# Kernel optimization log

Measured on AMD Instinct MI355X. Metric: run time of the kernel, lower is better.

Reference implementation:

```python
import jax, jax.numpy as jnp
import numpy as np

B, T, H, W, C = 8, 16, 64, 64, 16
HID = 64  # hidden_dim of each ConvLSTM cell
K = 3     # kernel size


def _convlstm_step(x, h, c, Wk, b):
    # conv over concat([x, h]) -> 4*HID gate channels (i, f, o, g)
    z = jax.lax.conv_general_dilated(
        jnp.concatenate([x, h], axis=-1), Wk,
        window_strides=(1, 1), padding='SAME',
        dimension_numbers=('NHWC', 'HWIO', 'NHWC')) + b
    i, f, o, g = jnp.split(z, 4, axis=-1)
    c_new = jax.nn.sigmoid(f) * c + jax.nn.sigmoid(i) * jnp.tanh(g)
    h_new = jax.nn.sigmoid(o) * jnp.tanh(c_new)
    return h_new, c_new


def setup_inputs() -> dict:
    key = jax.random.key(0)
    k1, k2, k3 = jax.random.split(key, 3)
    enc_input = jax.random.normal(k1, (B, T, H, W, C), jnp.float32)
    # input cell: in_channels = C + HID; stacked hidden cell: 2*HID
    W0 = jax.random.normal(k2, (K, K, C + HID, 4 * HID), jnp.float32) * 0.05
    b0 = jnp.zeros((4 * HID,), jnp.float32)
    W1 = jax.random.normal(k3, (K, K, 2 * HID, 4 * HID), jnp.float32) * 0.05
    b1 = jnp.zeros((4 * HID,), jnp.float32)
    return {"enc_input": enc_input, "W0": W0, "b0": b0, "W1": W1, "b1": b1}


def reference(enc_input, W0, b0, W1, b1):
    Bv, Tv, Hv, Wv, _ = enc_input.shape
    z0 = jnp.zeros((Bv, Hv, Wv, HID), enc_input.dtype)

    def step(carry, x_t):
        h0, c0, h1, c1 = carry
        h0, c0 = _convlstm_step(x_t, h0, c0, W0, b0)   # input ConvLSTM
        h1, c1 = _convlstm_step(h0, h1, c1, W1, b1)    # stacked hidden ConvLSTM
        return (h0, c0, h1, c1), None

    xs = jnp.moveaxis(enc_input, 1, 0)  # [T, B, H, W, C]
    (h0, c0, h1, c1), _ = jax.lax.scan(step, (z0, z0, z0, z0), xs)
    # Encoder returns last hidden layer's (h, c)
    return (h1, c1)
```

## Files before the change

kernel.cpp:

```cpp
#include <hip/hip_runtime.h>
#include <hip/hip_bf16.h>

#define Bv 8
#define Tv 16
#define Hv 64
#define Wv 64
#define Cv 16
#define HID 64
#define PH 66

typedef short short8 __attribute__((ext_vector_type(8)));
typedef float f32x4 __attribute__((ext_vector_type(4)));
typedef unsigned short u16x8 __attribute__((ext_vector_type(8)));

__device__ __forceinline__ unsigned short f2bf(float x) {
  union { float f; unsigned int u; } v; v.f = x;
  unsigned int r = v.u + 0x7FFF + ((v.u >> 16) & 1);
  return (unsigned short)(r >> 16);
}
__device__ __forceinline__ float sigmoid_f(float x) {
  return 1.f / (1.f + __expf(-x));
}
__device__ __forceinline__ float tanh_f(float x) {
  float e = __expf(2.f * x);
  return 1.f - 2.f / (e + 1.f);
}

__global__ void init_all(const float* __restrict__ enc,
                         const float* __restrict__ W0, const float* __restrict__ W1,
                         unsigned short* __restrict__ h0a, unsigned short* __restrict__ h0b,
                         unsigned short* __restrict__ h1a, unsigned short* __restrict__ h1b,
                         unsigned short* __restrict__ xb0, unsigned short* __restrict__ xb1,
                         unsigned short* __restrict__ w0r, unsigned short* __restrict__ w1r)
{
  const int gb = blockIdx.x, tid = threadIdx.x;
  if (gb < 293) {
    int idx = gb * 256 + tid;
    u16x8 z = {};
    if (idx < 8320) {
      int bufi = idx / 4160, rem = idx - bufi * 4160;
      int b = rem / 520, r2 = rem - b * 520;
      int hp = r2 >> 1, c8 = r2 & 1;
      int y, x;
      if (hp < 66)       { y = 0;  x = hp; }
      else if (hp < 132) { y = 65; x = hp - 66; }
      else { int i2 = hp - 132; y = 1 + (i2 >> 1); x = (i2 & 1) * 65; }
      unsigned short* base = bufi ? xb1 : xb0;
      *(u16x8*)(base + ((size_t)((b * PH + y) * PH) + x) * 16 + c8 * 8) = z;
      return;
    }
    idx -= 8320;
    int bufi = idx / 16640;
    if (bufi >= 4) return;
    int rem = idx - bufi * 16640;
    int b = rem / 2080, r2 = rem - b * 2080;
    int hp = r2 >> 3, c8 = r2 & 7;
    int y, x;
    if (hp < 66)       { y = 0;  x = hp; }
    else if (hp < 132) { y = 65; x = hp - 66; }
    else { int i2 = hp - 132; y = 1 + (i2 >> 1); x = (i2 & 1) * 65; }
    unsigned short* base = (bufi == 0) ? h0a : (bufi == 1) ? h0b : (bufi == 2) ? h1a : h1b;
    *(u16x8*)(base + ((size_t)((b * PH + y) * PH) + x) * 64 + c8 * 8) = z;
  } else if (gb < 1029) {
    int o = (gb - 293) * 256 + tid;
    if (o >= 23 * 8192) return;
    int cc = o >> 13, t = o & 8191;
    int wn = t >> 11, t2 = t & 2047;
    int g = t2 >> 9, t3 = t2 & 511;
    int l = t3 >> 3, e = t3 & 7;
    int kg = l >> 4, r = l & 15;
    int k = kg * 8 + e;
    int col = g * 64 + wn * 16 + r;
    float v = 0.f;
    if (cc < 4) {
      int tap = 2 * cc + (k >> 4);
      v = W0[(size_t)(tap * 80 + (k & 15)) * 256 + col];
    } else if (cc == 4) {
      if (k < 16) v = W0[(size_t)(8 * 80 + k) * 256 + col];
    } else {
      int hcc = cc - 5, tap = hcc >> 1, cgi = hcc & 1;
      v = W0[(size_t)(tap * 80 + 16 + cgi * 32 + k) * 256 + col];
    }
    w0r[o] = f2bf(v);
  } else if (gb < 2181) {
    int o = (gb - 1029) * 256 + tid;
    if (o >= 36 * 8192) return;
    int cc = o >> 13, t = o & 8191;
    int wn = t >> 11, t2 = t & 2047;
    int g = t2 >> 9, t3 = t2 & 511;
    int l = t3 >> 3, e = t3 & 7;
    int kg = l >> 4, r = l & 15;
    int k = kg * 8 + e;
    int col = g * 64 + wn * 16 + r;
    int tap = cc >> 2, cgi = cc & 3;
    w1r[o] = f2bf(W1[(size_t)(tap * 128 + cgi * 32 + k) * 256 + col]);
  } else {
    int idx = (gb - 2181) * 256 + tid;
    int b = idx >> 12, pix = idx & 4095;
    int y = pix >> 6, x = pix & 63;
    const float* s = enc + ((size_t)(b * Tv + 0) * 4096 + pix) * 16;
    float4 f0 = *(const float4*)(s);
    float4 f1 = *(const float4*)(s + 4);
    float4 f2 = *(const float4*)(s + 8);
    float4 f3 = *(const float4*)(s + 12);
    u16x8 o0, o1;
    o0[0]=f2bf(f0.x); o0[1]=f2bf(f0.y); o0[2]=f2bf(f0.z); o0[3]=f2bf(f0.w);
    o0[4]=f2bf(f1.x); o0[5]=f2bf(f1.y); o0[6]=f2bf(f1.z); o0[7]=f2bf(f1.w);
    o1[0]=f2bf(f2.x); o1[1]=f2bf(f2.y); o1[2]=f2bf(f2.z); o1[3]=f2bf(f2.w);
    o1[4]=f2bf(f3.x); o1[5]=f2bf(f3.y); o1[6]=f2bf(f3.z); o1[7]=f2bf(f3.w);
    unsigned short* d = xb0 + ((size_t)((b * PH + y + 1) * PH) + (x + 1)) * 16;
    *(u16x8*)(d)     = o0;
    *(u16x8*)(d + 8) = o1;
  }
}

template<int CELL, int NC>
__device__ __forceinline__ void cell_run(
    const char* __restrict__ A0, const char* __restrict__ A1,
    const char* __restrict__ Wr, const float* __restrict__ bias,
    float* __restrict__ cbuf, unsigned short* __restrict__ hout,
    float* __restrict__ h1fin, float* __restrict__ c1fin,
    char* lds, int b, int by, int bx, int tid)
{
  constexpr bool T0C = (CELL == 0) ? (NC == 5) : (NC == 18);
  const int l = tid & 63, w = tid >> 6;
  const int wm = w >> 2, wn = w & 3;
  const int r = l & 15, kg = l >> 4;
  const int j = wn * 16 + r;

  char* ldsA = lds;
  char* ldsW = lds + 3 * 8192;

  int pixs;
  {
    int ps = w * 16 + r;
    int ys = by * 16 + (ps >> 3), xs = bx * 8 + (ps & 7);
    pixs = (b * PH + ys) * PH + xs;
  }
  const int zpix = b * PH * PH;

  auto ISSUE_A = [&](int cc, int buf) {
    char* dst = ldsA + buf * 8192;
    if constexpr (CELL == 0) {
      if (cc < 5) {
        int tapA = 2 * cc;
        int kyA = tapA / 3, kxA = tapA - kyA * 3;
        unsigned offA = (unsigned)((pixs + kyA * PH + kxA) * 32 + kg * 16);
        unsigned offB;
        if (cc < 4) {
          int tapB = tapA + 1;
          int kyB = tapB / 3, kxB = tapB - kyB * 3;
          offB = (unsigned)((pixs + kyB * PH + kxB) * 32 + (kg - 2) * 16);
        } else {
          offB = (unsigned)(zpix * 32 + (kg - 2) * 16);
        }
        unsigned aoff = (kg < 2) ? offA : offB;
        __builtin_amdgcn_global_load_lds((const unsigned int*)(A0 + aoff),
                                         (unsigned int*)(dst + w * 1024), 16, 0, 0);
      } else {
        int hcc = cc - 5, tap = hcc >> 1, cgi = hcc & 1;
        int ky = tap / 3, kx = tap - ky * 3;
        unsigned aoff = (unsigned)((pixs + ky * PH + kx) * 128 + cgi * 64 + kg * 16);
        __builtin_amdgcn_global_load_lds((const unsigned int*)(A1 + aoff),
                                         (unsigned int*)(dst + w * 1024), 16, 0, 0);
      }
    } else {
      int tap, cgi;
      if (T0C) { tap = cc >> 1; cgi = cc & 1; }
      else     { tap = cc >> 2; cgi = cc & 3; }
      int ky = tap / 3, kx = tap - ky * 3;
      const char* srcb = (cgi < 2) ? A0 : A1;
      unsigned aoff = (unsigned)((pixs + ky * PH + kx) * 128 + (cgi & 1) * 64 + kg * 16);
      __builtin_amdgcn_global_load_lds((const unsigned int*)(srcb + aoff),
                                       (unsigned int*)(dst + w * 1024), 16, 0, 0);
    }
  };

  auto ISSUE_W = [&](int cc, int buf) {
    char* dst = ldsW + buf * 16384;
    int wcc;
    if constexpr (CELL == 0) wcc = cc;
    else                     wcc = T0C ? ((cc >> 1) * 4 + (cc & 1)) : cc;
    const char* wp = Wr + (size_t)wcc * 16384 + (unsigned)(w * 2048 + l * 16);
    __builtin_amdgcn_global_load_lds((const unsigned int*)(wp),
                                     (unsigned int*)(dst + w * 2048), 16, 0, 0);
    __builtin_amdgcn_global_load_lds((const unsigned int*)(wp + 1024),
                                     (unsigned int*)(dst + w * 2048 + 1024), 16, 0, 0);
  };

  f32x4 acc[4][4] = {};
  short8 af[4], bfv[4];

  ISSUE_W(0, 0);
  __builtin_amdgcn_sched_barrier(0);
  ISSUE_A(0, 0);
  __builtin_amdgcn_sched_barrier(0);
  ISSUE_A(1, 1);
  __builtin_amdgcn_sched_barrier(0);

#pragma unroll
  for (int cc = 0; cc < NC; ++cc) {
    if (cc == NC - 1) { asm volatile("s_waitcnt vmcnt(0)" ::: "memory"); }
    else              { asm volatile("s_waitcnt vmcnt(1)" ::: "memory"); }
    __builtin_amdgcn_sched_barrier(0);
    __builtin_amdgcn_s_barrier();
    __builtin_amdgcn_sched_barrier(0);

    if (cc + 1 < NC) ISSUE_W(cc + 1, (cc + 1) & 1);
    __builtin_amdgcn_sched_barrier(0);
    if (cc + 2 < NC) ISSUE_A(cc + 2, (cc + 2) % 3);

    const char* bufA = ldsA + (cc % 3) * 8192;
    const char* bufW = ldsW + (cc & 1) * 16384;
#pragma unroll
    for (int mi = 0; mi < 4; ++mi)
      af[mi] = *(const short8*)(bufA + (wm * 4 + mi) * 1024 + l * 16);
#pragma unroll
    for (int g = 0; g < 4; ++g)
      bfv[g] = *(const short8*)(bufW + (wn * 4 + g) * 1024 + l * 16);

    __builtin_amdgcn_s_setprio(1);
#pragma unroll
    for (int mi = 0; mi < 4; ++mi)
#pragma unroll
      for (int g = 0; g < 4; ++g)
        acc[mi][g] = __builtin_amdgcn_mfma_f32_16x16x32_bf16(
            af[mi], bfv[g], acc[mi][g], 0, 0, 0);
    __builtin_amdgcn_s_setprio(0);
  }

  float bi[4];
#pragma unroll
  for (int g = 0; g < 4; ++g) bi[g] = bias[g * 64 + j];
  float cpre[4][4];
#pragma unroll
  for (int mi = 0; mi < 4; ++mi) {
#pragma unroll
    for (int rg = 0; rg < 4; ++rg) {
      if constexpr (T0C) { cpre[mi][rg] = 0.f; }
      else {
        int p = wm * 64 + mi * 16 + kg * 4 + rg;
        int y = by * 16 + (p >> 3), x = bx * 8 + (p & 7);
        cpre[mi][rg] = cbuf[((size_t)((b * Hv + y) * Wv) + x) * HID + j];
      }
    }
  }
#pragma unroll
  for (int mi = 0; mi < 4; ++mi) {
#pragma unroll
    for (int rg = 0; rg < 4; ++rg) {
      int p = wm * 64 + mi * 16 + kg * 4 + rg;
      int y = by * 16 + (p >> 3), x = bx * 8 + (p & 7);
      float zi = acc[mi][0][rg] + bi[0];
      float zf = acc[mi][1][rg] + bi[1];
      float zo = acc[mi][2][rg] + bi[2];
      float zg = acc[mi][3][rg] + bi[3];
      float cn = sigmoid_f(zf) * cpre[mi][rg] + sigmoid_f(zi) * tanh_f(zg);
      float hn = sigmoid_f(zo) * tanh_f(cn);
      size_t ci = ((size_t)((b * Hv + y) * Wv) + x) * HID + j;
      cbuf[ci] = cn;
      hout[((size_t)((b * PH + y + 1) * PH) + (x + 1)) * HID + j] = f2bf(hn);
      if (CELL == 1 && h1fin != nullptr) {
        h1fin[ci] = hn;
        c1fin[ci] = cn;
      }
    }
  }
}

template<int NC1, int NC0, bool LAST>
__global__ __launch_bounds__(512, 4)
void step_fused(const unsigned short* __restrict__ xbr, unsigned short* __restrict__ xbw,
                const unsigned short* __restrict__ h0r, unsigned short* __restrict__ h0w,
                const unsigned short* __restrict__ h1r, unsigned short* __restrict__ h1w,
                const unsigned short* __restrict__ w0r, const unsigned short* __restrict__ w1r,
                const float* __restrict__ b0, const float* __restrict__ b1,
                float* __restrict__ c0, float* __restrict__ c1,
                float* __restrict__ h1f, float* __restrict__ c1f,
                const float* __restrict__ enc, int tnext)
{
  extern __shared__ char lds[];
  const int tid = threadIdx.x;
  const int gid = blockIdx.x;
  int isC1, k;
  if constexpr (NC1 > 0 && NC0 > 0) { isC1 = (gid < 256) ? 1 : 0; k = gid & 255; }
  else if constexpr (NC1 > 0)       { isC1 = 1; k = gid; }
  else                              { isC1 = 0; k = gid; }
  const int b = k >> 5, rem = k & 31;
  const int by = rem >> 3, bx = rem & 7;

  if constexpr (NC1 > 0) {
    if (isC1) {
      cell_run<1, NC1>((const char*)h0r, (const char*)h1r, (const char*)w1r, b1,
                       c1, h1w, LAST ? h1f : nullptr, LAST ? c1f : nullptr,
                       lds, b, by, bx, tid);
      return;
    }
  }
  if constexpr (NC0 > 0) {
    cell_run<0, NC0>((const char*)xbr, (const char*)h0r, (const char*)w0r, b0,
                     c0, h0w, nullptr, nullptr, lds, b, by, bx, tid);
    if (tnext >= 0) {
      int pp = tid >> 2, q4 = tid & 3;
      int y = by * 16 + (pp >> 3), x = bx * 8 + (pp & 7);
      const float* s = enc + ((size_t)(b * Tv + tnext) * 4096 + (y * 64 + x)) * 16 + q4 * 4;
      float4 f = *(const float4*)s;
      unsigned short* d = xbw + ((size_t)((b * PH + y + 1) * PH) + (x + 1)) * 16 + q4 * 4;
      d[0] = f2bf(f.x); d[1] = f2bf(f.y); d[2] = f2bf(f.z); d[3] = f2bf(f.w);
    }
  }
}

extern "C" void kernel_launch(void* const* d_in, const int* in_sizes, int n_in,
                              void* d_out, int out_size, void* d_ws, size_t ws_size,
                              hipStream_t stream) {
  const float* enc = (const float*)d_in[0];
  const float* W0  = (const float*)d_in[1];
  const float* b0  = (const float*)d_in[2];
  const float* W1  = (const float*)d_in[3];
  const float* b1  = (const float*)d_in[4];

  float* out = (float*)d_out;
  const size_t NST = (size_t)Bv * Hv * Wv * HID;
  float* h1f = out;
  float* c1  = out + NST;

  char* ws = (char*)d_ws;
  const size_t SZ_C = NST * 4;
  const size_t SZ_H = (size_t)Bv * PH * PH * HID * 2;
  const size_t SZ_X = (size_t)Bv * PH * PH * 16 * 2;
  float*          c0  = (float*)ws;
  unsigned short* h0a = (unsigned short*)(ws + SZ_C);
  unsigned short* h0b = (unsigned short*)(ws + SZ_C + SZ_H);
  unsigned short* h1a = (unsigned short*)(ws + SZ_C + 2 * SZ_H);
  unsigned short* h1b = (unsigned short*)(ws + SZ_C + 3 * SZ_H);
  unsigned short* xb0 = (unsigned short*)(ws + SZ_C + 4 * SZ_H);
  unsigned short* xb1 = (unsigned short*)(ws + SZ_C + 4 * SZ_H + SZ_X);
  unsigned short* w0r = (unsigned short*)(ws + SZ_C + 4 * SZ_H + 2 * SZ_X);
  unsigned short* w1r = (unsigned short*)(ws + SZ_C + 4 * SZ_H + 2 * SZ_X + (size_t)23 * 16384);

  hipFuncSetAttribute((const void*)step_fused<0,5,false>,   hipFuncAttributeMaxDynamicSharedMemorySize, 65536);
  hipFuncSetAttribute((const void*)step_fused<18,23,false>, hipFuncAttributeMaxDynamicSharedMemorySize, 65536);
  hipFuncSetAttribute((const void*)step_fused<36,23,false>, hipFuncAttributeMaxDynamicSharedMemorySize, 65536);
  hipFuncSetAttribute((const void*)step_fused<36,0,true>,   hipFuncAttributeMaxDynamicSharedMemorySize, 65536);

  init_all<<<2309, 256, 0, stream>>>(enc, W0, W1, h0a, h0b, h1a, h1b,
                                     xb0, xb1, w0r, w1r);

  const int LDSB = 57344;
  step_fused<0,5,false><<<256, 512, LDSB, stream>>>(
      xb0, xb1, h0b, h0a, h1a, h1b, w0r, w1r, b0, b1, c0, c1,
      nullptr, nullptr, enc, 1);
  for (int t = 1; t <= 15; ++t) {
    unsigned short* h0r = (t & 1) ? h0a : h0b;
    unsigned short* h0w = (t & 1) ? h0b : h0a;
    unsigned short* h1r = (t & 1) ? h1b : h1a;
    unsigned short* h1w = (t & 1) ? h1a : h1b;
    unsigned short* xr  = (t & 1) ? xb1 : xb0;
    unsigned short* xw  = (t & 1) ? xb0 : xb1;
    int tn = (t + 1 <= 15) ? (t + 1) : -1;
    if (t == 1)
      step_fused<18,23,false><<<512, 512, LDSB, stream>>>(
          xr, xw, h0r, h0w, h1r, h1w, w0r, w1r, b0, b1, c0, c1,
          nullptr, nullptr, enc, tn);
    else
      step_fused<36,23,false><<<512, 512, LDSB, stream>>>(
          xr, xw, h0r, h0w, h1r, h1w, w0r, w1r, b0, b1, c0, c1,
          nullptr, nullptr, enc, tn);
  }
  step_fused<36,0,true><<<256, 512, LDSB, stream>>>(
      xb0, xb1, h0b, h0a, h1a, h1b, w0r, w1r, b0, b1, c0, c1,
      h1f, c1, enc, -1);
}
```

Measured before the change: 604.1 us.

## Process two K-chunks per pipeline stage in stacked cell to halve barriers

Splits the cell routine into separate input-cell and hidden-cell versions. The hidden-cell version loads and computes two 32-channel chunks per pipeline stage with triple buffering, halving the number of barriers and waitcnt points per tap. This requires much larger LDS staging buffers, so the dynamic shared memory for every launch grows to 144 KB. That likely limits each CU to a single block and reduces latency hiding for both cells.

New measurement: 705.5 us. 16.8% more time.

```diff
diff --git a/kernel.cpp b/kernel.cpp
--- a/kernel.cpp
+++ b/kernel.cpp
@@ -114,15 +114,14 @@
   }
 }
 
-template<int CELL, int NC>
-__device__ __forceinline__ void cell_run(
+template<int NC>
+__device__ __forceinline__ void cell0_run(
     const char* __restrict__ A0, const char* __restrict__ A1,
     const char* __restrict__ Wr, const float* __restrict__ bias,
     float* __restrict__ cbuf, unsigned short* __restrict__ hout,
-    float* __restrict__ h1fin, float* __restrict__ c1fin,
     char* lds, int b, int by, int bx, int tid)
 {
-  constexpr bool T0C = (CELL == 0) ? (NC == 5) : (NC == 18);
+  constexpr bool T0C = (NC == 5);
   const int l = tid & 63, w = tid >> 6;
   const int wm = w >> 2, wn = w & 3;
   const int r = l & 15, kg = l >> 4;
@@ -141,47 +140,33 @@
 
   auto ISSUE_A = [&](int cc, int buf) {
     char* dst = ldsA + buf * 8192;
-    if constexpr (CELL == 0) {
-      if (cc < 5) {
-        int tapA = 2 * cc;
-        int kyA = tapA / 3, kxA = tapA - kyA * 3;
-        unsigned offA = (unsigned)((pixs + kyA * PH + kxA) * 32 + kg * 16);
-        unsigned offB;
-        if (cc < 4) {
-          int tapB = tapA + 1;
-          int kyB = tapB / 3, kxB = tapB - kyB * 3;
-          offB = (unsigned)((pixs + kyB * PH + kxB) * 32 + (kg - 2) * 16);
-        } else {
-          offB = (unsigned)(zpix * 32 + (kg - 2) * 16);
-        }
-        unsigned aoff = (kg < 2) ? offA : offB;
-        __builtin_amdgcn_global_load_lds((const unsigned int*)(A0 + aoff),
-                                         (unsigned int*)(dst + w * 1024), 16, 0, 0);
+    if (cc < 5) {
+      int tapA = 2 * cc;
+      int kyA = tapA / 3, kxA = tapA - kyA * 3;
+      unsigned offA = (unsigned)((pixs + kyA * PH + kxA) * 32 + kg * 16);
+      unsigned offB;
+      if (cc < 4) {
+        int tapB = tapA + 1;
+        int kyB = tapB / 3, kxB = tapB - kyB * 3;
+        offB = (unsigned)((pixs + kyB * PH + kxB) * 32 + (kg - 2) * 16);
       } else {
-        int hcc = cc - 5, tap = hcc >> 1, cgi = hcc & 1;
-        int ky = tap / 3, kx = tap - ky * 3;
-        unsigned aoff = (unsigned)((pixs + ky * PH + kx) * 128 + cgi * 64 + kg * 16);
-        __builtin_amdgcn_global_load_lds((const unsigned int*)(A1 + aoff),
-                                         (unsigned int*)(dst + w * 1024), 16, 0, 0);
+        offB = (unsigned)(zpix * 32 + (kg - 2) * 16);
       }
+      unsigned aoff = (kg < 2) ? offA : offB;
+      __builtin_amdgcn_global_load_lds((const unsigned int*)(A0 + aoff),
+                                       (unsigned int*)(dst + w * 1024), 16, 0, 0);
     } else {
-      int tap, cgi;
-      if (T0C) { tap = cc >> 1; cgi = cc & 1; }
-      else     { tap = cc >> 2; cgi = cc & 3; }
+      int hcc = cc - 5, tap = hcc >> 1, cgi = hcc & 1;
       int ky = tap / 3, kx = tap - ky * 3;
-      const char* srcb = (cgi < 2) ? A0 : A1;
-      unsigned aoff = (unsigned)((pixs + ky * PH + kx) * 128 + (cgi & 1) * 64 + kg * 16);
-      __builtin_amdgcn_global_load_lds((const unsigned int*)(srcb + aoff),
+      unsigned aoff = (unsigned)((pixs + ky * PH + kx) * 128 + cgi * 64 + kg * 16);
+      __builtin_amdgcn_global_load_lds((const unsigned int*)(A1 + aoff),
                                        (unsigned int*)(dst + w * 1024), 16, 0, 0);
     }
   };
 
   auto ISSUE_W = [&](int cc, int buf) {
     char* dst = ldsW + buf * 16384;
-    int wcc;
-    if constexpr (CELL == 0) wcc = cc;
-    else                     wcc = T0C ? ((cc >> 1) * 4 + (cc & 1)) : cc;
-    const char* wp = Wr + (size_t)wcc * 16384 + (unsigned)(w * 2048 + l * 16);
+    const char* wp = Wr + (size_t)cc * 16384 + (unsigned)(w * 2048 + l * 16);
     __builtin_amdgcn_global_load_lds((const unsigned int*)(wp),
                                      (unsigned int*)(dst + w * 2048), 16, 0, 0);
     __builtin_amdgcn_global_load_lds((const unsigned int*)(wp + 1024),
@@ -260,7 +245,126 @@
       size_t ci = ((size_t)((b * Hv + y) * Wv) + x) * HID + j;
       cbuf[ci] = cn;
       hout[((size_t)((b * PH + y + 1) * PH) + (x + 1)) * HID + j] = f2bf(hn);
-      if (CELL == 1 && h1fin != nullptr) {
+    }
+  }
+}
+
+template<int NC>
+__device__ __forceinline__ void cell1_run(
+    const char* __restrict__ A0, const char* __restrict__ A1,
+    const char* __restrict__ Wr, const float* __restrict__ bias,
+    float* __restrict__ cbuf, unsigned short* __restrict__ hout,
+    float* __restrict__ h1fin, float* __restrict__ c1fin,
+    char* lds, int b, int by, int bx, int tid)
+{
+  constexpr bool T0C = (NC == 18);
+  constexpr int NP = NC / 2;
+  const int l = tid & 63, w = tid >> 6;
+  const int wm = w >> 2, wn = w & 3;
+  const int r = l & 15, kg = l >> 4;
+  const int j = wn * 16 + r;
+
+  char* ldsA = lds;
+  char* ldsW = lds + 3 * 16384;
+
+  int pixs;
+  {
+    int ps = w * 16 + r;
+    int ys = by * 16 + (ps >> 3), xs = bx * 8 + (ps & 7);
+    pixs = (b * PH + ys) * PH + xs;
+  }
+
+  auto ISSUE = [&](int p, int buf) {
+    int tap, ss;
+    if (T0C) { tap = p; ss = 0; } else { tap = p >> 1; ss = p & 1; }
+    int ky = tap / 3, kx = tap - ky * 3;
+    const char* srcb = ss ? A1 : A0;
+    unsigned abase = (unsigned)((pixs + ky * PH + kx) * 128 + kg * 16);
+    char* dstA = ldsA + buf * 16384 + w * 1024;
+#pragma unroll
+    for (int hh = 0; hh < 2; ++hh)
+      __builtin_amdgcn_global_load_lds((const unsigned int*)(srcb + abase + hh * 64),
+                                       (unsigned int*)(dstA + hh * 8192), 16, 0, 0);
+    int wbase = tap * 4 + 2 * ss;
+    const char* wp = Wr + (size_t)wbase * 16384 + (unsigned)(w * 4096 + l * 16);
+    char* dstW = ldsW + buf * 32768 + w * 4096;
+#pragma unroll
+    for (int q = 0; q < 4; ++q)
+      __builtin_amdgcn_global_load_lds((const unsigned int*)(wp + q * 1024),
+                                       (unsigned int*)(dstW + q * 1024), 16, 0, 0);
+  };
+
+  f32x4 acc[4][4] = {};
+  short8 af[4], bfv[4];
+
+  ISSUE(0, 0);
+  __builtin_amdgcn_sched_barrier(0);
+  ISSUE(1, 1);
+  __builtin_amdgcn_sched_barrier(0);
+
+#pragma unroll
+  for (int p = 0; p < NP; ++p) {
+    if (p <= NP - 2) { asm volatile("s_waitcnt vmcnt(6)" ::: "memory"); }
+    else             { asm volatile("s_waitcnt vmcnt(0)" ::: "memory"); }
+    __builtin_amdgcn_sched_barrier(0);
+    __builtin_amdgcn_s_barrier();
+    __builtin_amdgcn_sched_barrier(0);
+
+    if (p + 2 < NP) ISSUE(p + 2, (p + 2) % 3);
+
+    const char* bufA = ldsA + (p % 3) * 16384;
+    const char* bufW = ldsW + (p % 3) * 32768;
+#pragma unroll
+    for (int s = 0; s < 2; ++s) {
+#pragma unroll
+      for (int mi = 0; mi < 4; ++mi)
+        af[mi] = *(const short8*)(bufA + s * 8192 + (wm * 4 + mi) * 1024 + l * 16);
+#pragma unroll
+      for (int g = 0; g < 4; ++g)
+        bfv[g] = *(const short8*)(bufW + s * 16384 + (wn * 4 + g) * 1024 + l * 16);
+      __builtin_amdgcn_s_setprio(1);
+#pragma unroll
+      for (int mi = 0; mi < 4; ++mi)
+#pragma unroll
+        for (int g = 0; g < 4; ++g)
+          acc[mi][g] = __builtin_amdgcn_mfma_f32_16x16x32_bf16(
+              af[mi], bfv[g], acc[mi][g], 0, 0, 0);
+      __builtin_amdgcn_s_setprio(0);
+    }
+  }
+
+  float bi[4];
+#pragma unroll
+  for (int g = 0; g < 4; ++g) bi[g] = bias[g * 64 + j];
+  float cpre[4][4];
+#pragma unroll
+  for (int mi = 0; mi < 4; ++mi) {
+#pragma unroll
+    for (int rg = 0; rg < 4; ++rg) {
+      if constexpr (T0C) { cpre[mi][rg] = 0.f; }
+      else {
+        int p = wm * 64 + mi * 16 + kg * 4 + rg;
+        int y = by * 16 + (p >> 3), x = bx * 8 + (p & 7);
+        cpre[mi][rg] = cbuf[((size_t)((b * Hv + y) * Wv) + x) * HID + j];
+      }
+    }
+  }
+#pragma unroll
+  for (int mi = 0; mi < 4; ++mi) {
+#pragma unroll
+    for (int rg = 0; rg < 4; ++rg) {
+      int p = wm * 64 + mi * 16 + kg * 4 + rg;
+      int y = by * 16 + (p >> 3), x = bx * 8 + (p & 7);
+      float zi = acc[mi][0][rg] + bi[0];
+      float zf = acc[mi][1][rg] + bi[1];
+      float zo = acc[mi][2][rg] + bi[2];
+      float zg = acc[mi][3][rg] + bi[3];
+      float cn = sigmoid_f(zf) * cpre[mi][rg] + sigmoid_f(zi) * tanh_f(zg);
+      float hn = sigmoid_f(zo) * tanh_f(cn);
+      size_t ci = ((size_t)((b * Hv + y) * Wv) + x) * HID + j;
+      cbuf[ci] = cn;
+      hout[((size_t)((b * PH + y + 1) * PH) + (x + 1)) * HID + j] = f2bf(hn);
+      if (h1fin != nullptr) {
         h1fin[ci] = hn;
         c1fin[ci] = cn;
       }
@@ -291,15 +395,15 @@
 
   if constexpr (NC1 > 0) {
     if (isC1) {
-      cell_run<1, NC1>((const char*)h0r, (const char*)h1r, (const char*)w1r, b1,
-                       c1, h1w, LAST ? h1f : nullptr, LAST ? c1f : nullptr,
-                       lds, b, by, bx, tid);
+      cell1_run<NC1>((const char*)h0r, (const char*)h1r, (const char*)w1r, b1,
+                     c1, h1w, LAST ? h1f : nullptr, LAST ? c1f : nullptr,
+                     lds, b, by, bx, tid);
       return;
     }
   }
   if constexpr (NC0 > 0) {
-    cell_run<0, NC0>((const char*)xbr, (const char*)h0r, (const char*)w0r, b0,
-                     c0, h0w, nullptr, nullptr, lds, b, by, bx, tid);
+    cell0_run<NC0>((const char*)xbr, (const char*)h0r, (const char*)w0r, b0,
+                   c0, h0w, lds, b, by, bx, tid);
     if (tnext >= 0) {
       int pp = tid >> 2, q4 = tid & 3;
       int y = by * 16 + (pp >> 3), x = bx * 8 + (pp & 7);
@@ -339,15 +443,15 @@
   unsigned short* w0r = (unsigned short*)(ws + SZ_C + 4 * SZ_H + 2 * SZ_X);
   unsigned short* w1r = (unsigned short*)(ws + SZ_C + 4 * SZ_H + 2 * SZ_X + (size_t)23 * 16384);
 
-  hipFuncSetAttribute((const void*)step_fused<0,5,false>,   hipFuncAttributeMaxDynamicSharedMemorySize, 65536);
-  hipFuncSetAttribute((const void*)step_fused<18,23,false>, hipFuncAttributeMaxDynamicSharedMemorySize, 65536);
-  hipFuncSetAttribute((const void*)step_fused<36,23,false>, hipFuncAttributeMaxDynamicSharedMemorySize, 65536);
-  hipFuncSetAttribute((const void*)step_fused<36,0,true>,   hipFuncAttributeMaxDynamicSharedMemorySize, 65536);
+  hipFuncSetAttribute((const void*)step_fused<0,5,false>,   hipFuncAttributeMaxDynamicSharedMemorySize, 147456);
+  hipFuncSetAttribute((const void*)step_fused<18,23,false>, hipFuncAttributeMaxDynamicSharedMemorySize, 147456);
+  hipFuncSetAttribute((const void*)step_fused<36,23,false>, hipFuncAttributeMaxDynamicSharedMemorySize, 147456);
+  hipFuncSetAttribute((const void*)step_fused<36,0,true>,   hipFuncAttributeMaxDynamicSharedMemorySize, 147456);
 
   init_all<<<2309, 256, 0, stream>>>(enc, W0, W1, h0a, h0b, h1a, h1b,
                                      xb0, xb1, w0r, w1r);
 
-  const int LDSB = 57344;
+  const int LDSB = 147456;
   step_fused<0,5,false><<<256, 512, LDSB, stream>>>(
       xb0, xb1, h0b, h0a, h1a, h1b, w0r, w1r, b0, b1, c0, c1,
       nullptr, nullptr, enc, 1);
```
